# Optimization experiments

Measured on AMD Instinct MI355X. Metric: run time of the kernel, lower is better.

The kernel has to match this reference:

```python
import jax, jax.numpy as jnp
import numpy as np

NEG_BIG = -9e15
ALPHA = 0.2  # leaky relu slope


def setup_inputs() -> dict:
    key = jax.random.key(0)
    k1, k2, k3, k4 = jax.random.split(key, 4)
    B, N, Fin, Fout = 8, 2048, 128, 64
    h = jax.random.normal(k1, (B, N, Fin), dtype=jnp.float32)
    adj = jax.random.randint(k2, (B, N, N), 0, 2, dtype=jnp.int32)
    # xavier_uniform-like init scale
    W = jax.random.uniform(k3, (Fin, Fout), dtype=jnp.float32, minval=-1.0, maxval=1.0) * (1.414 * np.sqrt(6.0 / (Fin + Fout)))
    a = jax.random.uniform(k4, (2 * Fout, 1), dtype=jnp.float32, minval=-1.0, maxval=1.0) * (1.414 * np.sqrt(6.0 / (2 * Fout + 1)))
    return {"h": h, "adj": adj, "W": W, "a": a}


def reference(h, adj, W, a):
    # h: [B,N,Fin], adj: [B,N,N], W: [Fin,Fout], a: [2*Fout,1]
    Fout = W.shape[1]
    Wh = jnp.einsum('bni,io->bno', h, W)            # [B,N,Fout]
    # e_ij = leakyrelu(a[:Fout] . Wh_i + a[Fout:] . Wh_j)  (decomposed, same math
    # as the original concat + matmul with a)
    f_src = Wh @ a[:Fout, 0]                        # [B,N]
    f_dst = Wh @ a[Fout:, 0]                        # [B,N]
    e = f_src[:, :, None] + f_dst[:, None, :]       # [B,N,N]
    e = jnp.where(e > 0, e, ALPHA * e)              # leaky relu
    e = jnp.where(adj > 0, e, NEG_BIG)              # mask
    attention = jax.nn.softmax(e, axis=2)           # [B,N,N]
    h_prime = jnp.einsum('bnm,bmo->bno', attention, Wh)
    return jax.nn.elu(h_prime)
```

## Files before the change

### kernel.cpp

```cpp
#include <hip/hip_runtime.h>
#include <hip/hip_bf16.h>

constexpr int Bb  = 8;
constexpr int Nn  = 2048;
constexpr int FIN = 128;
constexpr int FOUT = 64;

typedef __bf16 bf16x8 __attribute__((ext_vector_type(8)));
typedef float  f32x4  __attribute__((ext_vector_type(4)));
typedef int    i32x4  __attribute__((ext_vector_type(4)));

__device__ __forceinline__ unsigned int f2bf_bits(float f) {
    unsigned int u = __builtin_bit_cast(unsigned int, f);
    return (u + 0x7FFFu + ((u >> 16) & 1u)) >> 16;
}

__global__ __launch_bounds__(256) void gat_k1(
        const float* __restrict__ h, const float* __restrict__ W,
        const float* __restrict__ a, __bf16* __restrict__ whfrag,
        float* __restrict__ fs, float* __restrict__ fd) {
    const int blk = blockIdx.x;
    const int b   = blk >> 6;
    const int t32 = blk & 63;
    const int n0  = t32 * 32;
    const int l   = threadIdx.x & 63;
    const int w   = __builtin_amdgcn_readfirstlane((int)(threadIdx.x >> 6));

    const float a0 = a[l];
    const float a1 = a[FOUT + l];

    float acc[8];
#pragma unroll
    for (int r = 0; r < 8; ++r) acc[r] = 0.f;

    const float* hbase = h + (size_t)(b * Nn + n0 + w * 8) * FIN;

#pragma unroll 1
    for (int c0 = 0; c0 < FIN; c0 += 32) {
        float wreg[32];
#pragma unroll
        for (int cc = 0; cc < 32; ++cc) wreg[cc] = W[(c0 + cc) * FOUT + l];
#pragma unroll
        for (int r = 0; r < 8; ++r) {
            const float* hrow = hbase + r * FIN + c0;
#pragma unroll
            for (int cc = 0; cc < 32; ++cc) acc[r] = fmaf(hrow[cc], wreg[cc], acc[r]);
        }
    }

#pragma unroll
    for (int r = 0; r < 8; ++r) {
        float s0 = acc[r] * a0;
        float s1 = acc[r] * a1;
#pragma unroll
        for (int off = 32; off >= 1; off >>= 1) {
            s0 += __shfl_xor(s0, off, 64);
            s1 += __shfl_xor(s1, off, 64);
        }
        if (l == 0) {
            fs[b * Nn + n0 + w * 8 + r] = s0;
            fd[b * Nn + n0 + w * 8 + r] = s1;
        }
    }

    unsigned int pk[4];
#pragma unroll
    for (int i = 0; i < 4; ++i)
        pk[i] = f2bf_bits(acc[2 * i]) | (f2bf_bits(acc[2 * i + 1]) << 16);
    const int slotg = ((b * 64 + t32) * 4 + (l >> 4)) * 64 + ((w << 4) | (l & 15));
    reinterpret_cast<uint4*>(whfrag)[slotg] = make_uint4(pk[0], pk[1], pk[2], pk[3]);
}

__global__ __launch_bounds__(256, 4) void gat_k2(
        const int* __restrict__ adj, const __bf16* __restrict__ whfrag,
        const float* __restrict__ fs, const float* __restrict__ fd,
        float* __restrict__ out) {
    const int blk = blockIdx.x;
    const int b   = blk >> 7;
    const int i0  = (blk & 127) * 16;
    const int l   = threadIdx.x & 63;
    const int w   = __builtin_amdgcn_readfirstlane((int)(threadIdx.x >> 6));

    __shared__ __align__(16) char  aLDS[4 * 2048];
    __shared__ f32x4 comb[4][4][64];
    __shared__ float zpart[4][16];

    const int g  = l >> 4;
    const int jc = l & 15;

    char* myA = aLDS + w * 2048;

    float fs_loc[4];
#pragma unroll
    for (int rr = 0; rr < 4; ++rr) fs_loc[rr] = fs[b * Nn + i0 + g * 4 + rr];

    const int    jq0  = w * 512;
    const float* fdp  = fd + b * Nn + jq0 + jc * 4;
    const int*   adj0 = adj + (size_t)(b * Nn + i0 + g * 4) * Nn + jq0 + jc * 4;

    const bf16x8* bfr = reinterpret_cast<const bf16x8*>(whfrag)
                        + (size_t)((b * 64 + w * 16) * 4) * 64 + l;

    f32x4 acc[4] = {{0,0,0,0},{0,0,0,0},{0,0,0,0},{0,0,0,0}};
    float zp[4]  = {0.f, 0.f, 0.f, 0.f};

    i32x4 adjQ[2][4];
    f32x4 fdQ[2];

#pragma unroll
    for (int rr = 0; rr < 4; ++rr)
        adjQ[0][rr] = *reinterpret_cast<const i32x4*>(adj0 + (size_t)rr * Nn);
    fdQ[0] = *reinterpret_cast<const f32x4*>(fdp);

#pragma unroll
    for (int it = 0; it < 8; ++it) {
        const int cur = it & 1, nxt = cur ^ 1;
        if (it < 7) {
#pragma unroll
            for (int rr = 0; rr < 4; ++rr)
                adjQ[nxt][rr] = *reinterpret_cast<const i32x4*>(
                                    adj0 + (size_t)rr * Nn + (it + 1) * 64);
            fdQ[nxt] = *reinterpret_cast<const f32x4*>(fdp + (it + 1) * 64);
        }

#pragma unroll
        for (int rr = 0; rr < 4; ++rr) {
            const int row = g * 4 + rr;
            unsigned int wds[2];
#pragma unroll
            for (int hp = 0; hp < 2; ++hp) {
                unsigned int wd = 0;
#pragma unroll
                for (int q = 0; q < 2; ++q) {
                    const int jj = hp * 2 + q;
                    float e  = fs_loc[rr] + fdQ[cur][jj];
                    float lr = fmaxf(e, 0.2f * e);
                    float p  = exp2f(lr * 1.4426950408889634f);
                    p = (adjQ[cur][rr][jj] > 0) ? p : 0.f;
                    unsigned int pb = f2bf_bits(p);
                    zp[rr] += __builtin_bit_cast(float, pb << 16);
                    wd |= pb << (16 * q);
                }
                wds[hp] = wd;
            }
            const int boff = (row * 128 + jc * 8) ^ ((row & 7) << 4);
            *reinterpret_cast<uint2*>(myA + boff) = make_uint2(wds[0], wds[1]);
        }

#pragma unroll
        for (int kb = 0; kb < 2; ++kb) {
            const int rb = ((l & 15) * 128 + kb * 64 + g * 16) ^ ((l & 7) << 4);
            bf16x8 av = *reinterpret_cast<const bf16x8*>(myA + rb);
#pragma unroll
            for (int o16 = 0; o16 < 4; ++o16) {
                bf16x8 bv = bfr[((it * 2 + kb) * 4 + o16) * 64];
                acc[o16] = __builtin_amdgcn_mfma_f32_16x16x32_bf16(av, bv, acc[o16], 0, 0, 0);
            }
        }
    }

#pragma unroll
    for (int rr = 0; rr < 4; ++rr) {
#pragma unroll
        for (int off = 1; off <= 8; off <<= 1)
            zp[rr] += __shfl_xor(zp[rr], off, 64);
    }
    if (jc == 0) {
#pragma unroll
        for (int rr = 0; rr < 4; ++rr) zpart[w][g * 4 + rr] = zp[rr];
    }
#pragma unroll
    for (int o16 = 0; o16 < 4; ++o16) comb[w][o16][l] = acc[o16];
    __syncthreads();

    f32x4 res = comb[0][w][l];
#pragma unroll
    for (int wp = 1; wp < 4; ++wp) res += comb[wp][w][l];

#pragma unroll
    for (int r = 0; r < 4; ++r) {
        const int row = g * 4 + r;
        float z = zpart[0][row] + zpart[1][row] + zpart[2][row] + zpart[3][row];
        float v = res[r] / z;
        v = v > 0.f ? v : expm1f(v);
        out[(size_t)(b * Nn + i0 + row) * FOUT + w * 16 + jc] = v;
    }
}

extern "C" void kernel_launch(void* const* d_in, const int* in_sizes, int n_in,
                              void* d_out, int out_size, void* d_ws, size_t ws_size,
                              hipStream_t stream) {
    const float* h   = (const float*)d_in[0];
    const int*   adj = (const int*)d_in[1];
    const float* W   = (const float*)d_in[2];
    const float* a   = (const float*)d_in[3];
    float* out = (float*)d_out;

    __bf16* whfrag = (__bf16*)d_ws;
    float*  fs     = (float*)((char*)d_ws + (size_t)Bb * Nn * FOUT * 2);
    float*  fd     = fs + Bb * Nn;

    gat_k1<<<dim3(Bb * 64), dim3(256), 0, stream>>>(h, W, a, whfrag, fs, fd);
    gat_k2<<<dim3(Bb * 128), dim3(256), 0, stream>>>(adj, whfrag, fs, fd, out);
}
```

Before: 57.04 us.

## Double-buffer LDS attention tile, prefetch B fragments, fold log2e into scores

Folds the log2(e) scale into the fs/fd scores written by the first kernel, which removes a multiply per element in the softmax loop. The second kernel now ping-pongs the per-wave LDS attention tile between two buffers. It issues the global loads of Wh fragments early, before the exponent computation, and uses hardware bf16 conversion with a paired row-sum update. The loop unroll drops to 2, and an explicit lgkmcnt wait plus a sched_barrier constrain instruction scheduling. This doubles LDS use and adds register pressure from the prefetched fragments, which could reduce occupancy.

```diff
diff --git a/kernel.cpp b/kernel.cpp
--- a/kernel.cpp
+++ b/kernel.cpp
@@ -5,13 +5,16 @@
 constexpr int Nn  = 2048;
 constexpr int FIN = 128;
 constexpr int FOUT = 64;
+constexpr float LOG2E = 1.4426950408889634f;
 
 typedef __bf16 bf16x8 __attribute__((ext_vector_type(8)));
+typedef __bf16 bf16x2 __attribute__((ext_vector_type(2)));
 typedef float  f32x4  __attribute__((ext_vector_type(4)));
 typedef int    i32x4  __attribute__((ext_vector_type(4)));
-
-__device__ __forceinline__ unsigned int f2bf_bits(float f) {
-    unsigned int u = __builtin_bit_cast(unsigned int, f);
+typedef unsigned int u32;
+
+__device__ __forceinline__ u32 f2bf_bits(float f) {
+    u32 u = __builtin_bit_cast(u32, f);
     return (u + 0x7FFFu + ((u >> 16) & 1u)) >> 16;
 }
 
@@ -58,12 +61,12 @@
             s1 += __shfl_xor(s1, off, 64);
         }
         if (l == 0) {
-            fs[b * Nn + n0 + w * 8 + r] = s0;
-            fd[b * Nn + n0 + w * 8 + r] = s1;
-        }
-    }
-
-    unsigned int pk[4];
+            fs[b * Nn + n0 + w * 8 + r] = s0 * LOG2E;
+            fd[b * Nn + n0 + w * 8 + r] = s1 * LOG2E;
+        }
+    }
+
+    u32 pk[4];
 #pragma unroll
     for (int i = 0; i < 4; ++i)
         pk[i] = f2bf_bits(acc[2 * i]) | (f2bf_bits(acc[2 * i + 1]) << 16);
@@ -81,14 +84,14 @@
     const int l   = threadIdx.x & 63;
     const int w   = __builtin_amdgcn_readfirstlane((int)(threadIdx.x >> 6));
 
-    __shared__ __align__(16) char  aLDS[4 * 2048];
+    __shared__ __align__(16) char  aLDS[4 * 4096];
     __shared__ f32x4 comb[4][4][64];
     __shared__ float zpart[4][16];
 
     const int g  = l >> 4;
     const int jc = l & 15;
 
-    char* myA = aLDS + w * 2048;
+    char* myA = aLDS + w * 4096;
 
     float fs_loc[4];
 #pragma unroll
@@ -112,7 +115,7 @@
         adjQ[0][rr] = *reinterpret_cast<const i32x4*>(adj0 + (size_t)rr * Nn);
     fdQ[0] = *reinterpret_cast<const f32x4*>(fdp);
 
-#pragma unroll
+#pragma unroll 2
     for (int it = 0; it < 8; ++it) {
         const int cur = it & 1, nxt = cur ^ 1;
         if (it < 7) {
@@ -123,39 +126,58 @@
             fdQ[nxt] = *reinterpret_cast<const f32x4*>(fdp + (it + 1) * 64);
         }
 
+        bf16x8 bv0[4];
+#pragma unroll
+        for (int o16 = 0; o16 < 4; ++o16)
+            bv0[o16] = bfr[((it * 2 + 0) * 4 + o16) * 64];
+
+        char* buf = myA + cur * 2048;
 #pragma unroll
         for (int rr = 0; rr < 4; ++rr) {
             const int row = g * 4 + rr;
-            unsigned int wds[2];
+            u32 wds[2];
 #pragma unroll
             for (int hp = 0; hp < 2; ++hp) {
-                unsigned int wd = 0;
+                float pv[2];
 #pragma unroll
                 for (int q = 0; q < 2; ++q) {
                     const int jj = hp * 2 + q;
                     float e  = fs_loc[rr] + fdQ[cur][jj];
                     float lr = fmaxf(e, 0.2f * e);
-                    float p  = exp2f(lr * 1.4426950408889634f);
-                    p = (adjQ[cur][rr][jj] > 0) ? p : 0.f;
-                    unsigned int pb = f2bf_bits(p);
-                    zp[rr] += __builtin_bit_cast(float, pb << 16);
-                    wd |= pb << (16 * q);
+                    float p  = exp2f(lr);
+                    pv[q] = (adjQ[cur][rr][jj] > 0) ? p : 0.f;
                 }
+                u32 wd = __builtin_bit_cast(u32,
+                            (bf16x2){(__bf16)pv[0], (__bf16)pv[1]});
+                zp[rr] += __builtin_bit_cast(float, wd << 16);
+                zp[rr] += __builtin_bit_cast(float, wd & 0xffff0000u);
                 wds[hp] = wd;
             }
             const int boff = (row * 128 + jc * 8) ^ ((row & 7) << 4);
-            *reinterpret_cast<uint2*>(myA + boff) = make_uint2(wds[0], wds[1]);
-        }
-
-#pragma unroll
-        for (int kb = 0; kb < 2; ++kb) {
-            const int rb = ((l & 15) * 128 + kb * 64 + g * 16) ^ ((l & 7) << 4);
-            bf16x8 av = *reinterpret_cast<const bf16x8*>(myA + rb);
-#pragma unroll
-            for (int o16 = 0; o16 < 4; ++o16) {
-                bf16x8 bv = bfr[((it * 2 + kb) * 4 + o16) * 64];
-                acc[o16] = __builtin_amdgcn_mfma_f32_16x16x32_bf16(av, bv, acc[o16], 0, 0, 0);
-            }
+            *reinterpret_cast<uint2*>(buf + boff) = make_uint2(wds[0], wds[1]);
+        }
+
+        bf16x8 bv1[4];
+#pragma unroll
+        for (int o16 = 0; o16 < 4; ++o16)
+            bv1[o16] = bfr[((it * 2 + 1) * 4 + o16) * 64];
+
+        asm volatile("s_waitcnt lgkmcnt(0)" ::: "memory");
+        __builtin_amdgcn_sched_barrier(0);
+
+        {
+            const int rb0 = (((l & 15) * 128 + 0 * 64 + g * 16) ^ ((l & 7) << 4));
+            bf16x8 av = *reinterpret_cast<const bf16x8*>(buf + rb0);
+#pragma unroll
+            for (int o16 = 0; o16 < 4; ++o16)
+                acc[o16] = __builtin_amdgcn_mfma_f32_16x16x32_bf16(av, bv0[o16], acc[o16], 0, 0, 0);
+        }
+        {
+            const int rb1 = (((l & 15) * 128 + 1 * 64 + g * 16) ^ ((l & 7) << 4));
+            bf16x8 av = *reinterpret_cast<const bf16x8*>(buf + rb1);
+#pragma unroll
+            for (int o16 = 0; o16 < 4; ++o16)
+                acc[o16] = __builtin_amdgcn_mfma_f32_16x16x32_bf16(av, bv1[o16], acc[o16], 0, 0, 0);
         }
     }
 
```

Measured after the change: 52.52 us. 1.09x faster.
